# Performance work log

Hardware: AMD Instinct MI355X
Metric: run time of the kernel (lower is better)

Reference implementation:

```python
import jax, jax.numpy as jnp
import numpy as np


def _rotate_matrices(angles):
    # angles: (M, 1) -> rot (M, 2, 2), rows [[c, -s], [s, c]]
    c = jnp.cos(angles)
    s = jnp.sin(angles)
    rot = jnp.stack([jnp.concatenate([c, -s], axis=1),
                     jnp.concatenate([s, c], axis=1)], axis=1)
    return rot, jnp.swapaxes(rot, 1, 2)


def _seq_group_permute(x, mapping, perms, final=False):
    # x: (B, S, d), perms: (d//2, 2, 2)
    B, S, d = x.shape
    if not final:
        x = x[:, :, mapping]
    x = x.reshape(B, S, d // 2, 2)
    x = jnp.einsum('ijmk,mkn->ijmn', x, perms).reshape(B, S, d)
    if final:
        x = x[:, :, mapping]
    return x


def _mat_group_permute_inv(m, mapping, perms_inv, transposed):
    # m: (R, d), perms_inv: (d//2, 2, 2)
    R, d = m.shape
    m = m[:, mapping].reshape(R, d // 2, 2)
    sub = 'imk,mkn->imn' if transposed else 'imk,mnk->imn'
    return jnp.einsum(sub, m, perms_inv).reshape(R, d)


def setup_inputs() -> dict:
    key = jax.random.key(0)
    ks = jax.random.split(key, 8)
    B, S, IN, OUT = 4, 2048, 1024, 4096
    inp = jax.random.normal(ks[0], (B, S, IN), dtype=jnp.float32)
    weight = jax.random.normal(ks[1], (OUT, IN), dtype=jnp.float32) * 0.02
    mask = (jax.random.uniform(ks[2], (OUT, IN)) > 0.5).astype(jnp.float32)
    in_scores = jax.random.normal(ks[3], (IN // 2, 1), dtype=jnp.float32)
    out_scores = jax.random.normal(ks[4], (OUT // 2, 1), dtype=jnp.float32)
    in_mapping = jax.random.permutation(ks[5], IN).astype(jnp.int32)
    out_mapping = jax.random.permutation(ks[6], OUT).astype(jnp.int32)
    out_mapping_reverse = jnp.argsort(out_mapping).astype(jnp.int32)
    return {
        'input': inp,
        'weight': weight,
        'mask': mask,
        'in_permutation_scores': in_scores,
        'out_permutation_scores': out_scores,
        'in_mapping': in_mapping,
        'out_mapping': out_mapping,
        'out_mapping_reverse': out_mapping_reverse,
        'temperature': 1,
    }


def reference(input, weight, mask, in_permutation_scores, out_permutation_scores,
              in_mapping, out_mapping, out_mapping_reverse, temperature):
    in_permut, in_permut_inv = _rotate_matrices(in_permutation_scores)
    out_permut, out_permut_inv = _rotate_matrices(out_permutation_scores)
    # permute + rotate activations on the input side
    s_in = _seq_group_permute(input, in_mapping, in_permut)
    # inverse permute/rotate the weight's input dim, then its output dim
    m2 = _mat_group_permute_inv(weight, in_mapping, in_permut_inv, transposed=False)
    m3 = _mat_group_permute_inv(m2.T, out_mapping, out_permut_inv, transposed=True)
    m3 = m3 * mask.T  # (in, out)
    s_inner = jnp.einsum('bsi,io->bso', s_in, m3)
    s_out = _seq_group_permute(s_inner, out_mapping_reverse, out_permut, final=True)
    return s_out
```

## Files before the change

kernel.cpp:

```cpp
#include <hip/hip_runtime.h>
#include <hip/hip_bf16.h>
#include <stdint.h>

#define M_DIM 8192
#define K_DIM 1024
#define N_DIM 4096

typedef __bf16 bf16x8 __attribute__((ext_vector_type(8)));
typedef float  f32x4  __attribute__((ext_vector_type(4)));

__device__ __forceinline__ uint16_t f2bf(float f) {
  union { float f; uint32_t u; } x; x.f = f;
  uint32_t u = x.u;
  return (uint16_t)((u + 0x7FFFu + ((u >> 16) & 1u)) >> 16);
}

__global__ __launch_bounds__(256) void prologue_kernel(
    const float* __restrict__ input,
    const float* __restrict__ weight,
    const float* __restrict__ mask,
    const float* __restrict__ in_scores,
    const float* __restrict__ out_scores,
    const int*   __restrict__ in_mapping,
    const int*   __restrict__ out_mapping,
    uint16_t*    __restrict__ a_bf16,
    uint16_t*    __restrict__ w5t)
{
  __shared__ float    w0[K_DIM], w1[K_DIM];
  __shared__ uint16_t o0[K_DIM], o1[K_DIM];

  const int bid = blockIdx.x;
  const int t   = threadIdx.x;

  if (bid >= 2048) {
    const int i = (bid - 2048) * 256 + t;
    float4 v = ((const float4*)input)[i];
    ushort4 o;
    o.x = f2bf(v.x); o.y = f2bf(v.y); o.z = f2bf(v.z); o.w = f2bf(v.w);
    ((ushort4*)a_bf16)[i] = o;
    return;
  }

  const int mo = bid;

  const int r0 = out_mapping[2 * mo];
  const int r1 = out_mapping[2 * mo + 1];

  ((float4*)w0)[t] = ((const float4*)(weight + (size_t)r0 * K_DIM))[t];
  ((float4*)w1)[t] = ((const float4*)(weight + (size_t)r1 * K_DIM))[t];

  const float ao = out_scores[mo];
  const float so = sinf(ao), co = cosf(ao);

  __syncthreads();

#pragma unroll
  for (int s = 0; s < 2; s++) {
    const int mi = t + s * 256;
    const float ai = in_scores[mi];
    const float si = sinf(ai), ci = cosf(ai);
    const int ia0 = in_mapping[2 * mi];
    const int ia1 = in_mapping[2 * mi + 1];

    const float w00 = w0[ia0], w01 = w0[ia1];
    const float w10 = w1[ia0], w11 = w1[ia1];

    float a00 =  ci * w00 + si * w01;
    float a01 = -si * w00 + ci * w01;
    float a10 =  ci * w10 + si * w11;
    float a11 = -si * w10 + ci * w11;

    float b00 = co * a00 - so * a10;
    float b10 = co * a01 - so * a11;
    float b01 = so * a00 + co * a10;
    float b11 = so * a01 + co * a11;

    const float2 mk0 = *(const float2*)&mask[(size_t)(2 * mo) * K_DIM + 2 * mi];
    const float2 mk1 = *(const float2*)&mask[(size_t)(2 * mo + 1) * K_DIM + 2 * mi];
    b00 *= mk0.x; b10 *= mk0.y;
    b01 *= mk1.x; b11 *= mk1.y;

    float c00 =  co * b00 + so * b01;
    float c10 =  co * b10 + so * b11;
    float c01 = -so * b00 + co * b01;
    float c11 = -so * b10 + co * b11;

    o0[ia0] = f2bf(ci * c00 - si * c10);
    o0[ia1] = f2bf(si * c00 + ci * c10);
    o1[ia0] = f2bf(ci * c01 - si * c11);
    o1[ia1] = f2bf(si * c01 + ci * c11);
  }

  __syncthreads();

  ((uint2*)(w5t + (size_t)r0 * K_DIM))[t] = ((const uint2*)o0)[t];
  ((uint2*)(w5t + (size_t)r1 * K_DIM))[t] = ((const uint2*)o1)[t];
}

__device__ __forceinline__ void async_load16(const uint16_t* g, uint16_t* lds_wave_uniform) {
  __builtin_amdgcn_global_load_lds(
      (const __attribute__((address_space(1))) uint32_t*)g,
      (__attribute__((address_space(3))) uint32_t*)lds_wave_uniform,
      16, 0, 0);
}

__global__ __launch_bounds__(256, 2) void gemm_kernel(
    const uint16_t* __restrict__ A,
    const uint16_t* __restrict__ BT,
    float* __restrict__ C)
{
  __shared__ __align__(16) uint16_t As[2][256 * 32];
  __shared__ __align__(16) uint16_t Bs[2][128 * 32];

  const int tid  = threadIdx.x;
  const int w    = tid >> 6;
  const int lane = tid & 63;
  const int quad = lane >> 4;
  const int rr   = lane & 15;
  const int wm2  = w >> 1;
  const int wn2  = w & 1;

  const int flat = blockIdx.x;
  const int swz  = ((flat & 7) << 7) | (flat >> 3);
  const int bm   = swz >> 5;
  const int bn   = swz & 31;

  f32x4 acc[8][4] = {};

  const uint16_t* gA[4];
  const uint16_t* gB[2];
#pragma unroll
  for (int ii = 0; ii < 4; ii++) {
    const int c   = ii * 256 + tid;
    const int row = c >> 2;
    const int g   = (c & 3) ^ ((row >> 1) & 3);
    gA[ii] = A + (size_t)(bm * 256 + row) * K_DIM + g * 8;
  }
#pragma unroll
  for (int ii = 0; ii < 2; ii++) {
    const int c   = ii * 256 + tid;
    const int row = c >> 2;
    const int g   = (c & 3) ^ ((row >> 1) & 3);
    gB[ii] = BT + (size_t)(bn * 128 + row) * K_DIM + g * 8;
  }

#define STAGE(BUF, KT)                                                        \
  do {                                                                        \
    _Pragma("unroll")                                                         \
    for (int ii_ = 0; ii_ < 4; ii_++)                                         \
      async_load16(gA[ii_] + (KT) * 32, &As[BUF][(ii_ * 256 + w * 64) * 8]);  \
    _Pragma("unroll")                                                         \
    for (int ii_ = 0; ii_ < 2; ii_++)                                         \
      async_load16(gB[ii_] + (KT) * 32, &Bs[BUF][(ii_ * 256 + w * 64) * 8]);  \
  } while (0)

  int offA[8], offB[4];
#pragma unroll
  for (int i = 0; i < 8; i++) {
    const int r = wm2 * 128 + i * 16 + rr;
    offA[i] = (r * 4 + (quad ^ ((r >> 1) & 3))) * 8;
  }
#pragma unroll
  for (int j = 0; j < 4; j++) {
    const int r = wn2 * 64 + j * 16 + rr;
    offB[j] = (r * 4 + (quad ^ ((r >> 1) & 3))) * 8;
  }

#define TILE(T, MODE)                                                         \
  {                                                                           \
    const int buf_ = (T) & 1;                                                 \
    const uint16_t* asb_ = &As[buf_][0];                                      \
    const uint16_t* bsb_ = &Bs[buf_][0];                                      \
    bf16x8 af[8], bf[4];                                                      \
    _Pragma("unroll") for (int i_ = 0; i_ < 8; i_++)                          \
      af[i_] = *reinterpret_cast<const bf16x8*>(asb_ + offA[i_]);             \
    _Pragma("unroll") for (int j_ = 0; j_ < 4; j_++)                          \
      bf[j_] = *reinterpret_cast<const bf16x8*>(bsb_ + offB[j_]);             \
    asm volatile("s_waitcnt lgkmcnt(0)" ::: "memory");                        \
    __builtin_amdgcn_sched_barrier(0);      \
    __builtin_amdgcn_s_barrier();            \
    if (MODE == 0) STAGE(buf_, (T) + 2);                                      \
    __builtin_amdgcn_s_setprio(1);                                            \
    _Pragma("unroll") for (int i_ = 0; i_ < 8; i_++)                          \
      _Pragma("unroll") for (int j_ = 0; j_ < 4; j_++)                        \
        acc[i_][j_] = __builtin_amdgcn_mfma_f32_16x16x32_bf16(                \
            af[i_], bf[j_], acc[i_][j_], 0, 0, 0);                            \
    __builtin_amdgcn_s_setprio(0);                                            \
    if (MODE == 0)      { asm volatile("s_waitcnt vmcnt(6)" ::: "memory"); }  \
    else if (MODE == 1) { asm volatile("s_waitcnt vmcnt(0)" ::: "memory"); }  \
    if (MODE < 2) __builtin_amdgcn_s_barrier();                               \
  }

  STAGE(0, 0);
  STAGE(1, 1);
  asm volatile("s_waitcnt vmcnt(6)" ::: "memory");
  __builtin_amdgcn_s_barrier();

  for (int t = 0; t < 30; ++t) {
    TILE(t, 0);
  }
  TILE(30, 1);
  TILE(31, 2);

#undef TILE
#undef STAGE

#pragma unroll
  for (int i = 0; i < 8; i++) {
    const int row0 = bm * 256 + wm2 * 128 + i * 16 + quad * 4;
#pragma unroll
    for (int j = 0; j < 4; j++) {
      const int col = bn * 128 + wn2 * 64 + j * 16 + rr;
#pragma unroll
      for (int rg = 0; rg < 4; rg++) {
        C[(size_t)(row0 + rg) * N_DIM + col] = acc[i][j][rg];
      }
    }
  }
}

extern "C" void kernel_launch(void* const* d_in, const int* in_sizes, int n_in,
                              void* d_out, int out_size, void* d_ws, size_t ws_size,
                              hipStream_t stream) {
  const float* input      = (const float*)d_in[0];
  const float* weight     = (const float*)d_in[1];
  const float* mask       = (const float*)d_in[2];
  const float* in_scores  = (const float*)d_in[3];
  const float* out_scores = (const float*)d_in[4];
  const int*   in_mapping = (const int*)d_in[5];
  const int*   out_mapping= (const int*)d_in[6];
  float* out = (float*)d_out;

  uint16_t* a_bf16 = (uint16_t*)d_ws;
  uint16_t* w5t    = (uint16_t*)d_ws + (size_t)M_DIM * K_DIM;

  prologue_kernel<<<10240, 256, 0, stream>>>(
      input, weight, mask, in_scores, out_scores, in_mapping, out_mapping,
      a_bf16, w5t);

  gemm_kernel<<<1024, 256, 0, stream>>>(a_bf16, w5t, out);
}
```

Baseline: 254.3 us.

## Load B fragments directly to registers and deepen A LDS pipeline

The B operand is no longer staged through LDS. Each wave loads its B fragments straight from global memory into registers, double-buffered one tile ahead. The LDS freed by this goes to a 4-slot ring for A, prefetched three tiles ahead. The block-to-tile mapping also changes so each XCD works on a contiguous band of M rows. The intent is to cut LDS traffic and hide more global latency, at the cost of uncoalesced B register loads, more VGPR pressure and a more fragile wait-count schedule.

```diff
diff --git a/kernel.cpp b/kernel.cpp
--- a/kernel.cpp
+++ b/kernel.cpp
@@ -109,8 +109,7 @@
     const uint16_t* __restrict__ BT,
     float* __restrict__ C)
 {
-  __shared__ __align__(16) uint16_t As[2][256 * 32];
-  __shared__ __align__(16) uint16_t Bs[2][128 * 32];
+  __shared__ __align__(16) uint16_t As[4][256 * 32];
 
   const int tid  = threadIdx.x;
   const int w    = tid >> 6;
@@ -121,14 +120,14 @@
   const int wn2  = w & 1;
 
   const int flat = blockIdx.x;
-  const int swz  = ((flat & 7) << 7) | (flat >> 3);
-  const int bm   = swz >> 5;
-  const int bn   = swz & 31;
+  const int xcd  = flat & 7;
+  const int r_   = flat >> 3;
+  const int bn   = r_ >> 2;
+  const int bm   = xcd * 4 + (r_ & 3);
 
   f32x4 acc[8][4] = {};
 
   const uint16_t* gA[4];
-  const uint16_t* gB[2];
 #pragma unroll
   for (int ii = 0; ii < 4; ii++) {
     const int c   = ii * 256 + tid;
@@ -136,74 +135,78 @@
     const int g   = (c & 3) ^ ((row >> 1) & 3);
     gA[ii] = A + (size_t)(bm * 256 + row) * K_DIM + g * 8;
   }
-#pragma unroll
-  for (int ii = 0; ii < 2; ii++) {
-    const int c   = ii * 256 + tid;
-    const int row = c >> 2;
-    const int g   = (c & 3) ^ ((row >> 1) & 3);
-    gB[ii] = BT + (size_t)(bn * 128 + row) * K_DIM + g * 8;
-  }
-
-#define STAGE(BUF, KT)                                                        \
+
+  const uint16_t* gBf[4];
+#pragma unroll
+  for (int j = 0; j < 4; j++) {
+    const int rowb = bn * 128 + wn2 * 64 + j * 16 + rr;
+    gBf[j] = BT + (size_t)rowb * K_DIM + quad * 8;
+  }
+
+#define STAGE_A(SLOT, KT)                                                     \
   do {                                                                        \
     _Pragma("unroll")                                                         \
     for (int ii_ = 0; ii_ < 4; ii_++)                                         \
-      async_load16(gA[ii_] + (KT) * 32, &As[BUF][(ii_ * 256 + w * 64) * 8]);  \
+      async_load16(gA[ii_] + (KT) * 32, &As[SLOT][(ii_ * 256 + w * 64) * 8]); \
+  } while (0)
+
+#define LOAD_B(REG, KT)                                                       \
+  do {                                                                        \
     _Pragma("unroll")                                                         \
-    for (int ii_ = 0; ii_ < 2; ii_++)                                         \
-      async_load16(gB[ii_] + (KT) * 32, &Bs[BUF][(ii_ * 256 + w * 64) * 8]);  \
+    for (int j_ = 0; j_ < 4; j_++)                                            \
+      REG[j_] = *reinterpret_cast<const bf16x8*>(gBf[j_] + (KT) * 32);        \
   } while (0)
 
-  int offA[8], offB[4];
+  int offA[8];
 #pragma unroll
   for (int i = 0; i < 8; i++) {
     const int r = wm2 * 128 + i * 16 + rr;
     offA[i] = (r * 4 + (quad ^ ((r >> 1) & 3))) * 8;
   }
-#pragma unroll
-  for (int j = 0; j < 4; j++) {
-    const int r = wn2 * 64 + j * 16 + rr;
-    offB[j] = (r * 4 + (quad ^ ((r >> 1) & 3))) * 8;
-  }
-
-#define TILE(T, MODE)                                                         \
+
+#define TILE(T, BCUR, BNXT, DO_B, DO_ST, WMODE)                               \
   {                                                                           \
-    const int buf_ = (T) & 1;                                                 \
-    const uint16_t* asb_ = &As[buf_][0];                                      \
-    const uint16_t* bsb_ = &Bs[buf_][0];                                      \
-    bf16x8 af[8], bf[4];                                                      \
+    const uint16_t* asb_ = &As[(T) & 3][0];                                   \
+    bf16x8 af[8];                                                             \
     _Pragma("unroll") for (int i_ = 0; i_ < 8; i_++)                          \
       af[i_] = *reinterpret_cast<const bf16x8*>(asb_ + offA[i_]);             \
-    _Pragma("unroll") for (int j_ = 0; j_ < 4; j_++)                          \
-      bf[j_] = *reinterpret_cast<const bf16x8*>(bsb_ + offB[j_]);             \
+    if (DO_B) LOAD_B(BNXT, (T) + 1);                                          \
     asm volatile("s_waitcnt lgkmcnt(0)" ::: "memory");                        \
-    __builtin_amdgcn_sched_barrier(0);      \
-    __builtin_amdgcn_s_barrier();            \
-    if (MODE == 0) STAGE(buf_, (T) + 2);                                      \
+    __builtin_amdgcn_sched_barrier(0);                           \
+    __builtin_amdgcn_s_barrier();          \
+    if (DO_ST) STAGE_A(((T) + 3) & 3, (T) + 3);                               \
     __builtin_amdgcn_s_setprio(1);                                            \
     _Pragma("unroll") for (int i_ = 0; i_ < 8; i_++)                          \
       _Pragma("unroll") for (int j_ = 0; j_ < 4; j_++)                        \
         acc[i_][j_] = __builtin_amdgcn_mfma_f32_16x16x32_bf16(                \
-            af[i_], bf[j_], acc[i_][j_], 0, 0, 0);                            \
+            af[i_], BCUR[j_], acc[i_][j_], 0, 0, 0);                          \
     __builtin_amdgcn_s_setprio(0);                                            \
-    if (MODE == 0)      { asm volatile("s_waitcnt vmcnt(6)" ::: "memory"); }  \
-    else if (MODE == 1) { asm volatile("s_waitcnt vmcnt(0)" ::: "memory"); }  \
-    if (MODE < 2) __builtin_amdgcn_s_barrier();                               \
-  }
-
-  STAGE(0, 0);
-  STAGE(1, 1);
-  asm volatile("s_waitcnt vmcnt(6)" ::: "memory");
+    if (WMODE == 0)      { asm volatile("s_waitcnt vmcnt(4)" ::: "memory"); } \
+    else if (WMODE == 1) { asm volatile("s_waitcnt vmcnt(0)" ::: "memory"); } \
+    if (WMODE < 2) __builtin_amdgcn_s_barrier();                              \
+  }
+
+  bf16x8 bA[4], bB[4];
+
+  LOAD_B(bA, 0);
+  STAGE_A(0, 0);
+  STAGE_A(1, 1);
+  STAGE_A(2, 2);
+  asm volatile("s_waitcnt vmcnt(8)" ::: "memory");
   __builtin_amdgcn_s_barrier();
 
-  for (int t = 0; t < 30; ++t) {
-    TILE(t, 0);
-  }
-  TILE(30, 1);
-  TILE(31, 2);
+  for (int t = 0; t < 28; t += 2) {
+    TILE(t,     bA, bB, 1, 1, 0);
+    TILE(t + 1, bB, bA, 1, 1, 0);
+  }
+  TILE(28, bA, bB, 1, 1, 0);
+  TILE(29, bB, bA, 1, 0, 1);
+  TILE(30, bA, bB, 1, 0, 1);
+  TILE(31, bB, bA, 0, 0, 2);
 
 #undef TILE
-#undef STAGE
+#undef LOAD_B
+#undef STAGE_A
 
 #pragma unroll
   for (int i = 0; i < 8; i++) {
```

Result: slower. 281.1 us (+10.5%).

## Quantize activations and weights to int8 and use int8 MFMA GEMM

Applied to the files above, without the earlier changes.

Replaces the bf16 conversion and bf16 MFMA GEMM with per-row symmetric int8 quantization of the input and the transformed weight, then an int8 MFMA (16x16x64) GEMM with a dequantizing epilogue. The goal is to halve operand bytes and use the higher int8 matrix throughput, with half as many K-iterations. It adds a separate quantization kernel and scale arrays, and it loses numerical accuracy compared with bf16.

```diff
diff --git a/kernel.cpp b/kernel.cpp
--- a/kernel.cpp
+++ b/kernel.cpp
@@ -1,47 +1,67 @@
 #include <hip/hip_runtime.h>
-#include <hip/hip_bf16.h>
 #include <stdint.h>
 
 #define M_DIM 8192
 #define K_DIM 1024
 #define N_DIM 4096
 
-typedef __bf16 bf16x8 __attribute__((ext_vector_type(8)));
-typedef float  f32x4  __attribute__((ext_vector_type(4)));
-
-__device__ __forceinline__ uint16_t f2bf(float f) {
-  union { float f; uint32_t u; } x; x.f = f;
-  uint32_t u = x.u;
-  return (uint16_t)((u + 0x7FFFu + ((u >> 16) & 1u)) >> 16);
-}
-
-__global__ __launch_bounds__(256) void prologue_kernel(
+typedef int int32x4 __attribute__((ext_vector_type(4)));
+
+__device__ __forceinline__ uint32_t pack4(float a, float b, float c, float d, float inv) {
+  int q0 = (int)rintf(a * inv), q1 = (int)rintf(b * inv),
+      q2 = (int)rintf(c * inv), q3 = (int)rintf(d * inv);
+  q0 = q0 > 127 ? 127 : (q0 < -127 ? -127 : q0);
+  q1 = q1 > 127 ? 127 : (q1 < -127 ? -127 : q1);
+  q2 = q2 > 127 ? 127 : (q2 < -127 ? -127 : q2);
+  q3 = q3 > 127 ? 127 : (q3 < -127 ? -127 : q3);
+  return (uint32_t)(q0 & 255) | ((uint32_t)(q1 & 255) << 8) |
+         ((uint32_t)(q2 & 255) << 16) | ((uint32_t)(q3 & 255) << 24);
+}
+
+__global__ __launch_bounds__(256) void quant_a_kernel(
     const float* __restrict__ input,
+    int8_t*      __restrict__ a8,
+    float*       __restrict__ sA)
+{
+  const int wave = threadIdx.x >> 6, lane = threadIdx.x & 63;
+  const int row  = blockIdx.x * 4 + wave;
+  const float* rp = input + (size_t)row * K_DIM;
+
+  float4 v[4];
+  float m = 0.f;
+#pragma unroll
+  for (int j = 0; j < 4; j++) {
+    v[j] = ((const float4*)rp)[j * 64 + lane];
+    m = fmaxf(m, fmaxf(fmaxf(fabsf(v[j].x), fabsf(v[j].y)),
+                       fmaxf(fabsf(v[j].z), fabsf(v[j].w))));
+  }
+#pragma unroll
+  for (int off = 32; off >= 1; off >>= 1) m = fmaxf(m, __shfl_xor(m, off));
+
+  const float inv = (m > 0.f) ? 127.f / m : 0.f;
+  uint32_t* op = (uint32_t*)(a8 + (size_t)row * K_DIM);
+#pragma unroll
+  for (int j = 0; j < 4; j++)
+    op[j * 64 + lane] = pack4(v[j].x, v[j].y, v[j].z, v[j].w, inv);
+  if (lane == 0) sA[row] = m * (1.f / 127.f);
+}
+
+__global__ __launch_bounds__(256) void build_w_kernel(
     const float* __restrict__ weight,
     const float* __restrict__ mask,
     const float* __restrict__ in_scores,
     const float* __restrict__ out_scores,
     const int*   __restrict__ in_mapping,
     const int*   __restrict__ out_mapping,
-    uint16_t*    __restrict__ a_bf16,
-    uint16_t*    __restrict__ w5t)
+    int8_t*      __restrict__ w8,
+    float*       __restrict__ sW)
 {
-  __shared__ float    w0[K_DIM], w1[K_DIM];
-  __shared__ uint16_t o0[K_DIM], o1[K_DIM];
-
-  const int bid = blockIdx.x;
-  const int t   = threadIdx.x;
-
-  if (bid >= 2048) {
-    const int i = (bid - 2048) * 256 + t;
-    float4 v = ((const float4*)input)[i];
-    ushort4 o;
-    o.x = f2bf(v.x); o.y = f2bf(v.y); o.z = f2bf(v.z); o.w = f2bf(v.w);
-    ((ushort4*)a_bf16)[i] = o;
-    return;
-  }
-
-  const int mo = bid;
+  __shared__ float w0[K_DIM], w1[K_DIM];
+  __shared__ float o0f[K_DIM], o1f[K_DIM];
+  __shared__ float red[8];
+
+  const int mo = blockIdx.x;
+  const int t  = threadIdx.x;
 
   const int r0 = out_mapping[2 * mo];
   const int r1 = out_mapping[2 * mo + 1];
@@ -85,19 +105,41 @@
     float c01 = -so * b00 + co * b01;
     float c11 = -so * b10 + co * b11;
 
-    o0[ia0] = f2bf(ci * c00 - si * c10);
-    o0[ia1] = f2bf(si * c00 + ci * c10);
-    o1[ia0] = f2bf(ci * c01 - si * c11);
-    o1[ia1] = f2bf(si * c01 + ci * c11);
+    o0f[ia0] = ci * c00 - si * c10;
+    o0f[ia1] = si * c00 + ci * c10;
+    o1f[ia0] = ci * c01 - si * c11;
+    o1f[ia1] = si * c01 + ci * c11;
   }
 
   __syncthreads();
 
-  ((uint2*)(w5t + (size_t)r0 * K_DIM))[t] = ((const uint2*)o0)[t];
-  ((uint2*)(w5t + (size_t)r1 * K_DIM))[t] = ((const uint2*)o1)[t];
-}
-
-__device__ __forceinline__ void async_load16(const uint16_t* g, uint16_t* lds_wave_uniform) {
+  float m0 = 0.f, m1 = 0.f;
+#pragma unroll
+  for (int e = 0; e < 4; e++) {
+    m0 = fmaxf(m0, fabsf(o0f[4 * t + e]));
+    m1 = fmaxf(m1, fabsf(o1f[4 * t + e]));
+  }
+#pragma unroll
+  for (int off = 32; off >= 1; off >>= 1) {
+    m0 = fmaxf(m0, __shfl_xor(m0, off));
+    m1 = fmaxf(m1, __shfl_xor(m1, off));
+  }
+  if ((t & 63) == 0) { red[(t >> 6) * 2] = m0; red[(t >> 6) * 2 + 1] = m1; }
+  __syncthreads();
+  m0 = fmaxf(fmaxf(red[0], red[2]), fmaxf(red[4], red[6]));
+  m1 = fmaxf(fmaxf(red[1], red[3]), fmaxf(red[5], red[7]));
+
+  const float inv0 = (m0 > 0.f) ? 127.f / m0 : 0.f;
+  const float inv1 = (m1 > 0.f) ? 127.f / m1 : 0.f;
+
+  ((uint32_t*)(w8 + (size_t)r0 * K_DIM))[t] =
+      pack4(o0f[4 * t], o0f[4 * t + 1], o0f[4 * t + 2], o0f[4 * t + 3], inv0);
+  ((uint32_t*)(w8 + (size_t)r1 * K_DIM))[t] =
+      pack4(o1f[4 * t], o1f[4 * t + 1], o1f[4 * t + 2], o1f[4 * t + 3], inv1);
+  if (t == 0) { sW[r0] = m0 * (1.f / 127.f); sW[r1] = m1 * (1.f / 127.f); }
+}
+
+__device__ __forceinline__ void async_load16(const int8_t* g, int8_t* lds_wave_uniform) {
   __builtin_amdgcn_global_load_lds(
       (const __attribute__((address_space(1))) uint32_t*)g,
       (__attribute__((address_space(3))) uint32_t*)lds_wave_uniform,
@@ -105,12 +147,14 @@
 }
 
 __global__ __launch_bounds__(256, 2) void gemm_kernel(
-    const uint16_t* __restrict__ A,
-    const uint16_t* __restrict__ BT,
+    const int8_t* __restrict__ A,
+    const int8_t* __restrict__ BT,
+    const float*  __restrict__ sA,
+    const float*  __restrict__ sW,
     float* __restrict__ C)
 {
-  __shared__ __align__(16) uint16_t As[2][256 * 32];
-  __shared__ __align__(16) uint16_t Bs[2][128 * 32];
+  __shared__ __align__(16) int8_t As[2][256 * 64];
+  __shared__ __align__(16) int8_t Bs[2][128 * 64];
 
   const int tid  = threadIdx.x;
   const int w    = tid >> 6;
@@ -125,65 +169,65 @@
   const int bm   = swz >> 5;
   const int bn   = swz & 31;
 
-  f32x4 acc[8][4] = {};
-
-  const uint16_t* gA[4];
-  const uint16_t* gB[2];
+  int32x4 acc[8][4] = {};
+
+  const int8_t* gA[4];
+  const int8_t* gB[2];
 #pragma unroll
   for (int ii = 0; ii < 4; ii++) {
     const int c   = ii * 256 + tid;
     const int row = c >> 2;
     const int g   = (c & 3) ^ ((row >> 1) & 3);
-    gA[ii] = A + (size_t)(bm * 256 + row) * K_DIM + g * 8;
+    gA[ii] = A + (size_t)(bm * 256 + row) * K_DIM + g * 16;
   }
 #pragma unroll
   for (int ii = 0; ii < 2; ii++) {
     const int c   = ii * 256 + tid;
     const int row = c >> 2;
     const int g   = (c & 3) ^ ((row >> 1) & 3);
-    gB[ii] = BT + (size_t)(bn * 128 + row) * K_DIM + g * 8;
+    gB[ii] = BT + (size_t)(bn * 128 + row) * K_DIM + g * 16;
   }
 
 #define STAGE(BUF, KT)                                                        \
   do {                                                                        \
     _Pragma("unroll")                                                         \
     for (int ii_ = 0; ii_ < 4; ii_++)                                         \
-      async_load16(gA[ii_] + (KT) * 32, &As[BUF][(ii_ * 256 + w * 64) * 8]);  \
+      async_load16(gA[ii_] + (KT) * 64, &As[BUF][(ii_ * 256 + w * 64) * 16]); \
     _Pragma("unroll")                                                         \
     for (int ii_ = 0; ii_ < 2; ii_++)                                         \
-      async_load16(gB[ii_] + (KT) * 32, &Bs[BUF][(ii_ * 256 + w * 64) * 8]);  \
+      async_load16(gB[ii_] + (KT) * 64, &Bs[BUF][(ii_ * 256 + w * 64) * 16]); \
   } while (0)
 
   int offA[8], offB[4];
 #pragma unroll
   for (int i = 0; i < 8; i++) {
     const int r = wm2 * 128 + i * 16 + rr;
-    offA[i] = (r * 4 + (quad ^ ((r >> 1) & 3))) * 8;
+    offA[i] = r * 64 + (quad ^ ((r >> 1) & 3)) * 16;
   }
 #pragma unroll
   for (int j = 0; j < 4; j++) {
     const int r = wn2 * 64 + j * 16 + rr;
-    offB[j] = (r * 4 + (quad ^ ((r >> 1) & 3))) * 8;
+    offB[j] = r * 64 + (quad ^ ((r >> 1) & 3)) * 16;
   }
 
 #define TILE(T, MODE)                                                         \
   {                                                                           \
     const int buf_ = (T) & 1;                                                 \
-    const uint16_t* asb_ = &As[buf_][0];                                      \
-    const uint16_t* bsb_ = &Bs[buf_][0];                                      \
-    bf16x8 af[8], bf[4];                                                      \
+    const int8_t* asb_ = &As[buf_][0];                                        \
+    const int8_t* bsb_ = &Bs[buf_][0];                                        \
+    int32x4 af[8], bf[4];                                                     \
     _Pragma("unroll") for (int i_ = 0; i_ < 8; i_++)                          \
-      af[i_] = *reinterpret_cast<const bf16x8*>(asb_ + offA[i_]);             \
+      af[i_] = *reinterpret_cast<const int32x4*>(asb_ + offA[i_]);            \
     _Pragma("unroll") for (int j_ = 0; j_ < 4; j_++)                          \
-      bf[j_] = *reinterpret_cast<const bf16x8*>(bsb_ + offB[j_]);             \
+      bf[j_] = *reinterpret_cast<const int32x4*>(bsb_ + offB[j_]);            \
     asm volatile("s_waitcnt lgkmcnt(0)" ::: "memory");                        \
-    __builtin_amdgcn_sched_barrier(0);      \
+    __builtin_amdgcn_sched_barrier(0);                           \
     __builtin_amdgcn_s_barrier();            \
     if (MODE == 0) STAGE(buf_, (T) + 2);                                      \
     __builtin_amdgcn_s_setprio(1);                                            \
     _Pragma("unroll") for (int i_ = 0; i_ < 8; i_++)                          \
       _Pragma("unroll") for (int j_ = 0; j_ < 4; j_++)                        \
-        acc[i_][j_] = __builtin_amdgcn_mfma_f32_16x16x32_bf16(                \
+        acc[i_][j_] = __builtin_amdgcn_mfma_i32_16x16x64_i8(                  \
             af[i_], bf[j_], acc[i_][j_], 0, 0, 0);                            \
     __builtin_amdgcn_s_setprio(0);                                            \
     if (MODE == 0)      { asm volatile("s_waitcnt vmcnt(6)" ::: "memory"); }  \
@@ -196,24 +240,30 @@
   asm volatile("s_waitcnt vmcnt(6)" ::: "memory");
   __builtin_amdgcn_s_barrier();
 
-  for (int t = 0; t < 30; ++t) {
+  for (int t = 0; t < 14; ++t) {
     TILE(t, 0);
   }
-  TILE(30, 1);
-  TILE(31, 2);
+  TILE(14, 1);
+  TILE(15, 2);
 
 #undef TILE
 #undef STAGE
 
+  float sw4[4];
+#pragma unroll
+  for (int j = 0; j < 4; j++)
+    sw4[j] = sW[bn * 128 + wn2 * 64 + j * 16 + rr];
+
 #pragma unroll
   for (int i = 0; i < 8; i++) {
     const int row0 = bm * 256 + wm2 * 128 + i * 16 + quad * 4;
 #pragma unroll
-    for (int j = 0; j < 4; j++) {
-      const int col = bn * 128 + wn2 * 64 + j * 16 + rr;
-#pragma unroll
-      for (int rg = 0; rg < 4; rg++) {
-        C[(size_t)(row0 + rg) * N_DIM + col] = acc[i][j][rg];
+    for (int rg = 0; rg < 4; rg++) {
+      const float sa = sA[row0 + rg];
+#pragma unroll
+      for (int j = 0; j < 4; j++) {
+        const int col = bn * 128 + wn2 * 64 + j * 16 + rr;
+        C[(size_t)(row0 + rg) * N_DIM + col] = (float)acc[i][j][rg] * sa * sw4[j];
       }
     }
   }
@@ -231,12 +281,15 @@
   const int*   out_mapping= (const int*)d_in[6];
   float* out = (float*)d_out;
 
-  uint16_t* a_bf16 = (uint16_t*)d_ws;
-  uint16_t* w5t    = (uint16_t*)d_ws + (size_t)M_DIM * K_DIM;
-
-  prologue_kernel<<<10240, 256, 0, stream>>>(
-      input, weight, mask, in_scores, out_scores, in_mapping, out_mapping,
-      a_bf16, w5t);
-
-  gemm_kernel<<<1024, 256, 0, stream>>>(a_bf16, w5t, out);
-}
+  int8_t* a8 = (int8_t*)d_ws;
+  int8_t* w8 = (int8_t*)d_ws + (size_t)M_DIM * K_DIM;
+  float*  sA = (float*)((char*)d_ws + 12 * 1024 * 1024);
+  float*  sW = (float*)((char*)d_ws + 12 * 1024 * 1024 + 32 * 1024);
+
+  quant_a_kernel<<<2048, 256, 0, stream>>>(input, a8, sA);
+
+  build_w_kernel<<<2048, 256, 0, stream>>>(
+      weight, mask, in_scores, out_scores, in_mapping, out_mapping, w8, sW);
+
+  gemm_kernel<<<1024, 256, 0, stream>>>(a8, w8, sA, sW, out);
+}
```

New measurement: 227.9 us. 1.12x faster.
